# Kernel tuning notes

Hardware: AMD Instinct MI355X
Metric: run time of the kernel (lower is better)

Reference implementation:

```python
import jax, jax.numpy as jnp
import numpy as np

B, T, H, OUT = 256, 512, 512, 256  # batch, seq_len, hidden_size, out_seq_len


def setup_inputs() -> dict:
    key = jax.random.key(0)
    ks = jax.random.split(key, 16)
    sc = 1.0 / np.sqrt(H)  # torch GRU/Linear uniform(-1/sqrt(H),1/sqrt(H)) scale; use scaled normal
    p = lambda k, shape: (jax.random.normal(k, shape, jnp.float32) * sc)
    return {
        "x": jax.random.normal(ks[0], (B, T, 1), jnp.float32),
        # GRU layer 0 (input size 1)
        "W_ih0": p(ks[1], (3 * H, 1)),
        "W_hh0": p(ks[2], (3 * H, H)),
        "b_ih0": p(ks[3], (3 * H,)),
        "b_hh0": p(ks[4], (3 * H,)),
        # GRU layer 1 (input size H)
        "W_ih1": p(ks[5], (3 * H, H)),
        "W_hh1": p(ks[6], (3 * H, H)),
        "b_ih1": p(ks[7], (3 * H,)),
        "b_hh1": p(ks[8], (3 * H,)),
        # FC head: Linear(H,H)+ReLU, Linear(H,H)+ReLU, Linear(H,OUT)+Sigmoid
        "W1": p(ks[9], (H, H)),  "b1": p(ks[10], (H,)),
        "W2": p(ks[11], (H, H)), "b2": p(ks[12], (H,)),
        "W3": p(ks[13], (OUT, H)), "b3": p(ks[14], (OUT,)),
    }


def gru_layer(x, Wih, Whh, bih, bhh):
    # x: [B, T, in]; torch GRU equations (gate order r, z, n)
    gx = jnp.einsum('bti,gi->btg', x, Wih) + bih  # [B, T, 3H], input part precomputed

    def step(h, g):
        gh = h @ Whh.T + bhh                      # [B, 3H]
        xr, xz, xn = jnp.split(g, 3, axis=-1)
        hr, hz, hn = jnp.split(gh, 3, axis=-1)
        r = jax.nn.sigmoid(xr + hr)
        z = jax.nn.sigmoid(xz + hz)
        n = jnp.tanh(xn + r * hn)
        h = (1.0 - z) * n + z * h
        return h, h

    h0 = jnp.zeros((x.shape[0], Whh.shape[1]), x.dtype)
    _, hs = jax.lax.scan(step, h0, jnp.swapaxes(gx, 0, 1))  # [T, B, H]
    return jnp.swapaxes(hs, 0, 1)                            # [B, T, H]


def reference(x, W_ih0, W_hh0, b_ih0, b_hh0, W_ih1, W_hh1, b_ih1, b_hh1,
              W1, b1, W2, b2, W3, b3):
    h = gru_layer(x, W_ih0, W_hh0, b_ih0, b_hh0)
    h = gru_layer(h, W_ih1, W_hh1, b_ih1, b_hh1)
    y = h[:, -1]                                  # last timestep, [B, H]
    y = jax.nn.relu(y @ W1.T + b1)
    y = jax.nn.relu(y @ W2.T + b2)
    y = jax.nn.sigmoid(y @ W3.T + b3)             # [B, OUT]
    return y[..., None]                            # [B, OUT, 1]
```

## Files before the change

### kernel.cpp

```cpp
#include <hip/hip_runtime.h>


#define HSLOT 131072

typedef __attribute__((ext_vector_type(8))) _Float16 f16x8;
typedef __attribute__((ext_vector_type(4))) float f32x4;

__device__ __forceinline__ float sig_(float v) { return 1.0f / (1.0f + expf(-v)); }

__global__ __launch_bounds__(256) void ws_zero_v4(float* __restrict__ h) {
  int i = blockIdx.x * 256 + threadIdx.x;
  for (; i < 4 * HSLOT; i += gridDim.x * 256) h[i] = 0.f;
}

__global__ __launch_bounds__(256) void gru_step_m(
    const float* __restrict__ x,
    const float* __restrict__ Wih0, const float* __restrict__ bih0,
    const float* __restrict__ Whh0, const float* __restrict__ bhh0,
    const float* __restrict__ Wih1, const float* __restrict__ bih1,
    const float* __restrict__ Whh1, const float* __restrict__ bhh1,
    float* __restrict__ h0, float* __restrict__ h1, const int t)
{
  extern __shared__ char lds[];
  const int tid = threadIdx.x;
  const int w = tid >> 6, lane = tid & 63, l15 = lane & 15, q = lane >> 4;
  const bool isL1 = blockIdx.x >= 128;
  const int bb2 = isL1 ? (int)blockIdx.x - 128 : (int)blockIdx.x;
  const int bt = bb2 & 3, dt = bb2 >> 2;
  if (!isL1 && t >= 512) return;
  if (isL1 && t < 1) return;
  const int m0 = bt * 64;
  const int d  = dt * 16 + l15;

  const float* h0prev = h0 + (size_t)((t + 1) & 1) * HSLOT;

  {
    const int NR = isL1 ? 96 : 48;
    for (int u = tid; u < NR * 64; u += 256) {
      const int r = u >> 6, c8 = u & 63;
      const int mat = r >> 6 >= 0 ? (r >= 48 ? 1 : 0) : 0;
      const int rr = r - mat * 48, g3 = rr >> 4, dd = rr & 15;
      const float* W = isL1 ? (mat ? Whh1 : Wih1) : Whh0;
      const float* src = W + (size_t)(g3 * 512 + dt * 16 + dd) * 512 + (c8 << 3);
      const float4 v0 = *(const float4*)src;
      const float4 v1 = *(const float4*)(src + 4);
      f16x8 hv;
      hv[0] = (_Float16)v0.x; hv[1] = (_Float16)v0.y;
      hv[2] = (_Float16)v0.z; hv[3] = (_Float16)v0.w;
      hv[4] = (_Float16)v1.x; hv[5] = (_Float16)v1.y;
      hv[6] = (_Float16)v1.z; hv[7] = (_Float16)v1.w;
      *(f16x8*)(lds + (r << 10) + ((c8 ^ (r & 7)) << 4)) = hv;
    }
  }
  __syncthreads();

  f32x4 acc[6];
  #pragma unroll
  for (int i = 0; i < 6; ++i) acc[i] = (f32x4){0.f, 0.f, 0.f, 0.f};

  const float* h1prev = h1 + (size_t)(t & 1) * HSLOT;
  const size_t arow = (size_t)(m0 + w * 16 + l15) * 512 + (q << 3);

  #pragma unroll
  for (int half = 0; half < 2; ++half) {
    f16x8 a0[8], a1[8];
    #pragma unroll
    for (int kc2 = 0; kc2 < 8; ++kc2) {
      const int kc = half * 8 + kc2;
      const float* ap0 = h0prev + arow + kc * 32;
      const float4 u0 = *(const float4*)ap0, u1 = *(const float4*)(ap0 + 4);
      a0[kc2][0] = (_Float16)u0.x; a0[kc2][1] = (_Float16)u0.y;
      a0[kc2][2] = (_Float16)u0.z; a0[kc2][3] = (_Float16)u0.w;
      a0[kc2][4] = (_Float16)u1.x; a0[kc2][5] = (_Float16)u1.y;
      a0[kc2][6] = (_Float16)u1.z; a0[kc2][7] = (_Float16)u1.w;
      if (isL1) {
        const float* ap1 = h1prev + arow + kc * 32;
        const float4 v0 = *(const float4*)ap1, v1 = *(const float4*)(ap1 + 4);
        a1[kc2][0] = (_Float16)v0.x; a1[kc2][1] = (_Float16)v0.y;
        a1[kc2][2] = (_Float16)v0.z; a1[kc2][3] = (_Float16)v0.w;
        a1[kc2][4] = (_Float16)v1.x; a1[kc2][5] = (_Float16)v1.y;
        a1[kc2][6] = (_Float16)v1.z; a1[kc2][7] = (_Float16)v1.w;
      }
    }
    #pragma unroll
    for (int kc2 = 0; kc2 < 8; ++kc2) {
      const int kc = half * 8 + kc2;
      const int bb = ((kc << 6) + (q << 4)) ^ ((l15 & 7) << 4);
      #pragma unroll
      for (int g3 = 0; g3 < 3; ++g3) {
        const f16x8 bf = *(const f16x8*)(lds + ((g3 * 16 + l15) << 10) + bb);
        acc[g3] = __builtin_amdgcn_mfma_f32_16x16x32_f16(a0[kc2], bf, acc[g3], 0, 0, 0);
      }
      if (isL1) {
        #pragma unroll
        for (int g3 = 0; g3 < 3; ++g3) {
          const f16x8 bf = *(const f16x8*)(lds + 49152 + ((g3 * 16 + l15) << 10) + bb);
          acc[3 + g3] = __builtin_amdgcn_mfma_f32_16x16x32_f16(a1[kc2], bf, acc[3 + g3], 0, 0, 0);
        }
      }
    }
  }

  if (!isL1) {
    const float wxr = Wih0[d], wxz = Wih0[512 + d], wxn = Wih0[1024 + d];
    const float bxr = bih0[d], bxz = bih0[512 + d], bxn = bih0[1024 + d];
    const float bhr = bhh0[d], bhz = bhh0[512 + d], bhn = bhh0[1024 + d];
    float* hdst = h0 + (size_t)(t & 1) * HSLOT;
    #pragma unroll
    for (int j = 0; j < 4; ++j) {
      const int b = m0 + w * 16 + q * 4 + j;
      const float xv = x[(size_t)b * 512 + t];
      const float hp = h0prev[(size_t)b * 512 + d];
      const float r = sig_(xv * wxr + bxr + acc[0][j] + bhr);
      const float z = sig_(xv * wxz + bxz + acc[1][j] + bhz);
      const float n = tanhf(xv * wxn + bxn + r * (acc[2][j] + bhn));
      hdst[(size_t)b * 512 + d] = (1.f - z) * n + z * hp;
    }
  } else {
    const float bxr = bih1[d], bxz = bih1[512 + d], bxn = bih1[1024 + d];
    const float bhr = bhh1[d], bhz = bhh1[512 + d], bhn = bhh1[1024 + d];
    float* hdst = h1 + (size_t)((t + 1) & 1) * HSLOT;
    #pragma unroll
    for (int j = 0; j < 4; ++j) {
      const int b = m0 + w * 16 + q * 4 + j;
      const float hp = h1prev[(size_t)b * 512 + d];
      const float r = sig_(acc[0][j] + bxr + acc[3][j] + bhr);
      const float z = sig_(acc[1][j] + bxz + acc[4][j] + bhz);
      const float n = tanhf(acc[2][j] + bxn + r * (acc[5][j] + bhn));
      hdst[(size_t)b * 512 + d] = (1.f - z) * n + z * hp;
    }
  }
}

__global__ __launch_bounds__(256)
void mlp_head_v4(const float* __restrict__ X, const float* __restrict__ W,
                 const float* __restrict__ bias, float* __restrict__ Y,
                 const int N, const int act)
{
  __shared__ float Xs[32][258];
  __shared__ float Ws[8][260];
  const int tid = threadIdx.x;
  const int m0 = blockIdx.x << 5;
  const int j0 = blockIdx.y << 6;
  const int b  = tid >> 3;
  const int jj = tid & 7;
  float acc[8];
  #pragma unroll
  for (int i = 0; i < 8; ++i) acc[i] = 0.f;
  for (int kh = 0; kh < 2; ++kh) {
    __syncthreads();
    for (int u = tid; u < 2048; u += 256) {
      const int row = u >> 6, c4 = u & 63;
      const float4 v = *((const float4*)(X + ((m0 + row) << 9) + (kh << 8)) + c4);
      float* dst = &Xs[row][c4 << 2];
      dst[0] = v.x; dst[1] = v.y; dst[2] = v.z; dst[3] = v.w;
    }
    __syncthreads();
    #pragma unroll
    for (int jg = 0; jg < 8; ++jg) {
      if (jg) __syncthreads();
      for (int u = tid; u < 512; u += 256) {
        const int row = u >> 6, c4 = u & 63;
        const float4 v = *((const float4*)(W + ((j0 + (jg << 3) + row) << 9) + (kh << 8)) + c4);
        float* dst = &Ws[row][c4 << 2];
        dst[0] = v.x; dst[1] = v.y; dst[2] = v.z; dst[3] = v.w;
      }
      __syncthreads();
      float a = 0.f;
      #pragma unroll 8
      for (int k = 0; k < 256; ++k) a += Xs[b][k] * Ws[jj][k];
      acc[jg] += a;
    }
  }
  #pragma unroll
  for (int jg = 0; jg < 8; ++jg) {
    const int j = j0 + (jg << 3) + jj;
    float v = acc[jg] + bias[j];
    v = act ? (1.f / (1.f + __expf(-v))) : fmaxf(v, 0.f);
    Y[(m0 + b) * N + j] = v;
  }
}

extern "C" void kernel_launch(void* const* d_in, const int* in_sizes, int n_in,
                              void* d_out, int out_size, void* d_ws, size_t ws_size,
                              hipStream_t stream) {
  (void)in_sizes; (void)n_in; (void)out_size; (void)ws_size;
  const float* x    = (const float*)d_in[0];
  const float* Wih0 = (const float*)d_in[1];
  const float* Whh0 = (const float*)d_in[2];
  const float* bih0 = (const float*)d_in[3];
  const float* bhh0 = (const float*)d_in[4];
  const float* Wih1 = (const float*)d_in[5];
  const float* Whh1 = (const float*)d_in[6];
  const float* bih1 = (const float*)d_in[7];
  const float* bhh1 = (const float*)d_in[8];
  const float* W1 = (const float*)d_in[9];
  const float* b1 = (const float*)d_in[10];
  const float* W2 = (const float*)d_in[11];
  const float* b2 = (const float*)d_in[12];
  const float* W3 = (const float*)d_in[13];
  const float* b3 = (const float*)d_in[14];

  float* h0 = (float*)d_ws;
  float* h1 = h0 + 2 * HSLOT;
  float* y1 = h1 + 2 * HSLOT;
  float* y2 = y1 + HSLOT;

  hipFuncSetAttribute((const void*)gru_step_m,
                      hipFuncAttributeMaxDynamicSharedMemorySize, 98304);

  ws_zero_v4<<<64, 256, 0, stream>>>(h0);
  for (int t = 0; t <= 512; ++t)
    gru_step_m<<<256, 256, 98304, stream>>>(x, Wih0, bih0, Whh0, bhh0,
                                            Wih1, bih1, Whh1, bhh1, h0, h1, t);
  mlp_head_v4<<<dim3(8, 8), 256, 0, stream>>>(h1 + HSLOT, W1, b1, y1, 512, 0);
  mlp_head_v4<<<dim3(8, 8), 256, 0, stream>>>(y1, W2, b2, y2, 512, 0);
  mlp_head_v4<<<dim3(8, 4), 256, 0, stream>>>(y2, W3, b3, (float*)d_out, 256, 1);
}
```

Measured before the change: 10.81 ms.

## Replace per-timestep launches with persistent cooperative GRU kernel and grid barrier

Swaps 513 separate step launches for one cooperative persistent kernel of 192 blocks, each synchronised per timestep by a hierarchical atomic grid barrier. Work is split into three roles: layer0 recurrence, layer1 input projection (pipelined one step ahead through a gx buffer), and layer1 recurrence. Weights stay resident in LDS across all steps and hidden state is kept in registers, while the exchanged state is stored as fp16, which halves state traffic and removes conversions. The risks are the latency of a spin barrier on every step and extra fp16 rounding of the shared hidden state.

```diff
diff --git a/kernel.cpp b/kernel.cpp
--- a/kernel.cpp
+++ b/kernel.cpp
@@ -1,47 +1,56 @@
 #include <hip/hip_runtime.h>
 
 
-#define HSLOT 131072
+#define NTH 512
 
 typedef __attribute__((ext_vector_type(8))) _Float16 f16x8;
 typedef __attribute__((ext_vector_type(4))) float f32x4;
 
+__device__ __forceinline__ unsigned short f2h(float f) {
+  union { _Float16 h; unsigned short u; } v; v.h = (_Float16)f;
+  return v.u;
+}
 __device__ __forceinline__ float sig_(float v) { return 1.0f / (1.0f + expf(-v)); }
 
-__global__ __launch_bounds__(256) void ws_zero_v4(float* __restrict__ h) {
+__global__ __launch_bounds__(256) void ws_zero_v5(unsigned* __restrict__ p) {
   int i = blockIdx.x * 256 + threadIdx.x;
-  for (; i < 4 * HSLOT; i += gridDim.x * 256) h[i] = 0.f;
-}
-
-__global__ __launch_bounds__(256) void gru_step_m(
+  for (; i < 262144; i += gridDim.x * 256) p[i] = 0u;
+}
+
+__global__ __launch_bounds__(NTH, 1) void gru_persist(
     const float* __restrict__ x,
-    const float* __restrict__ Wih0, const float* __restrict__ bih0,
-    const float* __restrict__ Whh0, const float* __restrict__ bhh0,
-    const float* __restrict__ Wih1, const float* __restrict__ bih1,
-    const float* __restrict__ Whh1, const float* __restrict__ bhh1,
-    float* __restrict__ h0, float* __restrict__ h1, const int t)
+    const float* __restrict__ Wih0, const float* __restrict__ Whh0,
+    const float* __restrict__ bih0, const float* __restrict__ bhh0,
+    const float* __restrict__ Wih1, const float* __restrict__ Whh1,
+    const float* __restrict__ bih1, const float* __restrict__ bhh1,
+    char* __restrict__ ws, float* __restrict__ h1f)
 {
   extern __shared__ char lds[];
+
+  unsigned* cnt = (unsigned*)ws;
+  unsigned* gen = (unsigned*)(ws + 512);
+  unsigned short* h0b = (unsigned short*)(ws + 4096);
+  unsigned short* h1b = h0b + 2 * 131072;
+  float* gxb = (float*)(ws + 1052672);
+
   const int tid = threadIdx.x;
-  const int w = tid >> 6, lane = tid & 63, l15 = lane & 15, q = lane >> 4;
-  const bool isL1 = blockIdx.x >= 128;
-  const int bb2 = isL1 ? (int)blockIdx.x - 128 : (int)blockIdx.x;
-  const int bt = bb2 & 3, dt = bb2 >> 2;
-  if (!isL1 && t >= 512) return;
-  if (isL1 && t < 1) return;
-  const int m0 = bt * 64;
-  const int d  = dt * 16 + l15;
-
-  const float* h0prev = h0 + (size_t)((t + 1) & 1) * HSLOT;
+  const int wv = tid >> 6, lane = tid & 63, l15 = lane & 15, q = lane >> 4;
+  const int bid = blockIdx.x;
+  const int role = bid >> 6;
+  const int rb = bid & 63;
+  const int bt = rb & 3, dt = rb >> 2;
+  const int rg = wv >> 1;
+  const int hh = wv & 1;
+  const int row0 = bt * 64 + rg * 16;
+  const int dim = dt * 32 + hh * 16 + l15;
+  const int swl = (l15 & 7) << 4;
 
   {
-    const int NR = isL1 ? 96 : 48;
-    for (int u = tid; u < NR * 64; u += 256) {
+    const float* Wsrc = role == 0 ? Whh0 : (role == 1 ? Wih1 : Whh1);
+    for (int u = tid; u < 96 * 64; u += NTH) {
       const int r = u >> 6, c8 = u & 63;
-      const int mat = r >> 6 >= 0 ? (r >= 48 ? 1 : 0) : 0;
-      const int rr = r - mat * 48, g3 = rr >> 4, dd = rr & 15;
-      const float* W = isL1 ? (mat ? Whh1 : Wih1) : Whh0;
-      const float* src = W + (size_t)(g3 * 512 + dt * 16 + dd) * 512 + (c8 << 3);
+      const int g3 = r >> 5, dd = r & 31;
+      const float* src = Wsrc + (size_t)((g3 << 9) + dt * 32 + dd) * 512 + (c8 << 3);
       const float4 v0 = *(const float4*)src;
       const float4 v1 = *(const float4*)(src + 4);
       f16x8 hv;
@@ -52,88 +61,127 @@
       *(f16x8*)(lds + (r << 10) + ((c8 ^ (r & 7)) << 4)) = hv;
     }
   }
+
+  float c0w[3], c0i[3], c0h[3], c1i[3], c1h[3];
+  if (role == 0) {
+    #pragma unroll
+    for (int g3 = 0; g3 < 3; ++g3) {
+      c0w[g3] = Wih0[(g3 << 9) + dim];
+      c0i[g3] = bih0[(g3 << 9) + dim];
+      c0h[g3] = bhh0[(g3 << 9) + dim];
+    }
+  } else if (role == 2) {
+    #pragma unroll
+    for (int g3 = 0; g3 < 3; ++g3) {
+      c1i[g3] = bih1[(g3 << 9) + dim];
+      c1h[g3] = bhh1[(g3 << 9) + dim];
+    }
+  }
+
+  float hst[4];
+  #pragma unroll
+  for (int j = 0; j < 4; ++j) hst[j] = 0.f;
+
   __syncthreads();
 
-  f32x4 acc[6];
-  #pragma unroll
-  for (int i = 0; i < 6; ++i) acc[i] = (f32x4){0.f, 0.f, 0.f, 0.f};
-
-  const float* h1prev = h1 + (size_t)(t & 1) * HSLOT;
-  const size_t arow = (size_t)(m0 + w * 16 + l15) * 512 + (q << 3);
-
-  #pragma unroll
-  for (int half = 0; half < 2; ++half) {
-    f16x8 a0[8], a1[8];
-    #pragma unroll
-    for (int kc2 = 0; kc2 < 8; ++kc2) {
-      const int kc = half * 8 + kc2;
-      const float* ap0 = h0prev + arow + kc * 32;
-      const float4 u0 = *(const float4*)ap0, u1 = *(const float4*)(ap0 + 4);
-      a0[kc2][0] = (_Float16)u0.x; a0[kc2][1] = (_Float16)u0.y;
-      a0[kc2][2] = (_Float16)u0.z; a0[kc2][3] = (_Float16)u0.w;
-      a0[kc2][4] = (_Float16)u1.x; a0[kc2][5] = (_Float16)u1.y;
-      a0[kc2][6] = (_Float16)u1.z; a0[kc2][7] = (_Float16)u1.w;
-      if (isL1) {
-        const float* ap1 = h1prev + arow + kc * 32;
-        const float4 v0 = *(const float4*)ap1, v1 = *(const float4*)(ap1 + 4);
-        a1[kc2][0] = (_Float16)v0.x; a1[kc2][1] = (_Float16)v0.y;
-        a1[kc2][2] = (_Float16)v0.z; a1[kc2][3] = (_Float16)v0.w;
-        a1[kc2][4] = (_Float16)v1.x; a1[kc2][5] = (_Float16)v1.y;
-        a1[kc2][6] = (_Float16)v1.z; a1[kc2][7] = (_Float16)v1.w;
-      }
-    }
-    #pragma unroll
-    for (int kc2 = 0; kc2 < 8; ++kc2) {
-      const int kc = half * 8 + kc2;
-      const int bb = ((kc << 6) + (q << 4)) ^ ((l15 & 7) << 4);
+  for (int t = 0; t <= 513; ++t) {
+    const bool act = (role == 0) ? (t < 512)
+                   : (role == 1) ? (t >= 1 && t <= 512)
+                                 : (t >= 2);
+    f32x4 acc[3];
+    #pragma unroll
+    for (int g3 = 0; g3 < 3; ++g3) acc[g3] = (f32x4){0.f, 0.f, 0.f, 0.f};
+
+    if (act) {
+      const unsigned short* hsrc =
+          (role == 2 ? h1b : h0b) + (size_t)((t + 1) & 1) * 131072;
+      const unsigned short* ap = hsrc + (size_t)(row0 + l15) * 512 + (q << 3);
       #pragma unroll
-      for (int g3 = 0; g3 < 3; ++g3) {
-        const f16x8 bf = *(const f16x8*)(lds + ((g3 * 16 + l15) << 10) + bb);
-        acc[g3] = __builtin_amdgcn_mfma_f32_16x16x32_f16(a0[kc2], bf, acc[g3], 0, 0, 0);
-      }
-      if (isL1) {
-        #pragma unroll
-        for (int g3 = 0; g3 < 3; ++g3) {
-          const f16x8 bf = *(const f16x8*)(lds + 49152 + ((g3 * 16 + l15) << 10) + bb);
-          acc[3 + g3] = __builtin_amdgcn_mfma_f32_16x16x32_f16(a1[kc2], bf, acc[3 + g3], 0, 0, 0);
+      for (int half = 0; half < 2; ++half) {
+        f16x8 af[8];
+        #pragma unroll
+        for (int kc2 = 0; kc2 < 8; ++kc2)
+          af[kc2] = *(const f16x8*)(ap + (half * 8 + kc2) * 32);
+        #pragma unroll
+        for (int kc2 = 0; kc2 < 8; ++kc2) {
+          const int kc = half * 8 + kc2;
+          const int bb = ((kc << 6) + (q << 4)) ^ swl;
+          #pragma unroll
+          for (int g3 = 0; g3 < 3; ++g3) {
+            const f16x8 bf = *(const f16x8*)(lds + (((g3 << 5) + (hh << 4) + l15) << 10) + bb);
+            acc[g3] = __builtin_amdgcn_mfma_f32_16x16x32_f16(af[kc2], bf, acc[g3], 0, 0, 0);
+          }
         }
       }
     }
-  }
-
-  if (!isL1) {
-    const float wxr = Wih0[d], wxz = Wih0[512 + d], wxn = Wih0[1024 + d];
-    const float bxr = bih0[d], bxz = bih0[512 + d], bxn = bih0[1024 + d];
-    const float bhr = bhh0[d], bhz = bhh0[512 + d], bhn = bhh0[1024 + d];
-    float* hdst = h0 + (size_t)(t & 1) * HSLOT;
-    #pragma unroll
-    for (int j = 0; j < 4; ++j) {
-      const int b = m0 + w * 16 + q * 4 + j;
-      const float xv = x[(size_t)b * 512 + t];
-      const float hp = h0prev[(size_t)b * 512 + d];
-      const float r = sig_(xv * wxr + bxr + acc[0][j] + bhr);
-      const float z = sig_(xv * wxz + bxz + acc[1][j] + bhz);
-      const float n = tanhf(xv * wxn + bxn + r * (acc[2][j] + bhn));
-      hdst[(size_t)b * 512 + d] = (1.f - z) * n + z * hp;
-    }
-  } else {
-    const float bxr = bih1[d], bxz = bih1[512 + d], bxn = bih1[1024 + d];
-    const float bhr = bhh1[d], bhz = bhh1[512 + d], bhn = bhh1[1024 + d];
-    float* hdst = h1 + (size_t)((t + 1) & 1) * HSLOT;
-    #pragma unroll
-    for (int j = 0; j < 4; ++j) {
-      const int b = m0 + w * 16 + q * 4 + j;
-      const float hp = h1prev[(size_t)b * 512 + d];
-      const float r = sig_(acc[0][j] + bxr + acc[3][j] + bhr);
-      const float z = sig_(acc[1][j] + bxz + acc[4][j] + bhz);
-      const float n = tanhf(acc[2][j] + bxn + r * (acc[5][j] + bhn));
-      hdst[(size_t)b * 512 + d] = (1.f - z) * n + z * hp;
-    }
+
+    if (act) {
+      if (role == 0) {
+        unsigned short* hdst = h0b + (size_t)(t & 1) * 131072;
+        #pragma unroll
+        for (int j = 0; j < 4; ++j) {
+          const int row = row0 + q * 4 + j;
+          const float xv = x[(size_t)row * 512 + t];
+          const float r = sig_(xv * c0w[0] + c0i[0] + acc[0][j] + c0h[0]);
+          const float z = sig_(xv * c0w[1] + c0i[1] + acc[1][j] + c0h[1]);
+          const float n = tanhf(xv * c0w[2] + c0i[2] + r * (acc[2][j] + c0h[2]));
+          const float h = (1.f - z) * n + z * hst[j];
+          hst[j] = h;
+          hdst[(size_t)row * 512 + dim] = f2h(h);
+        }
+      } else if (role == 1) {
+        float* gxc = gxb + (size_t)(((t + 1) & 1) * 64 + rb) * 6144;
+        #pragma unroll
+        for (int g3 = 0; g3 < 3; ++g3)
+          #pragma unroll
+          for (int j = 0; j < 4; ++j)
+            gxc[(rg * 16 + q * 4 + j) * 96 + (g3 << 5) + (hh << 4) + l15] = acc[g3][j];
+      } else {
+        const float* gxc = gxb + (size_t)((t & 1) * 64 + rb) * 6144;
+        unsigned short* hdst = h1b + (size_t)(t & 1) * 131072;
+        #pragma unroll
+        for (int j = 0; j < 4; ++j) {
+          const int rr = rg * 16 + q * 4 + j;
+          const float gxr = gxc[rr * 96 + (hh << 4) + l15];
+          const float gxz = gxc[rr * 96 + 32 + (hh << 4) + l15];
+          const float gxn = gxc[rr * 96 + 64 + (hh << 4) + l15];
+          const float r = sig_(gxr + c1i[0] + acc[0][j] + c1h[0]);
+          const float z = sig_(gxz + c1i[1] + acc[1][j] + c1h[1]);
+          const float n = tanhf(gxn + c1i[2] + r * (acc[2][j] + c1h[2]));
+          const float h = (1.f - z) * n + z * hst[j];
+          hst[j] = h;
+          const int row = row0 + q * 4 + j;
+          hdst[(size_t)row * 512 + dim] = f2h(h);
+          if (t == 513) h1f[(size_t)row * 512 + dim] = h;
+        }
+      }
+    }
+
+    __syncthreads();
+    if (tid == 0) {
+      __hip_atomic_fetch_add(&cnt[(bid & 7) << 4], 1u,
+                             __ATOMIC_RELEASE, __HIP_MEMORY_SCOPE_AGENT);
+      const unsigned tgt = 24u * (unsigned)(t + 1);
+      if (bid == 0) {
+        for (int i = 0; i < 8; ++i)
+          while (__hip_atomic_load(&cnt[i << 4], __ATOMIC_ACQUIRE,
+                                   __HIP_MEMORY_SCOPE_AGENT) < tgt)
+            __builtin_amdgcn_s_sleep(2);
+        __hip_atomic_store(gen, (unsigned)(t + 1),
+                           __ATOMIC_RELEASE, __HIP_MEMORY_SCOPE_AGENT);
+      } else {
+        while (__hip_atomic_load(gen, __ATOMIC_ACQUIRE,
+                                 __HIP_MEMORY_SCOPE_AGENT) < (unsigned)(t + 1))
+          __builtin_amdgcn_s_sleep(2);
+      }
+    }
+    __syncthreads();
+    __builtin_amdgcn_sched_barrier(0);
   }
 }
 
 __global__ __launch_bounds__(256)
-void mlp_head_v4(const float* __restrict__ X, const float* __restrict__ W,
+void mlp_head_v5(const float* __restrict__ X, const float* __restrict__ W,
                  const float* __restrict__ bias, float* __restrict__ Y,
                  const int N, const int act)
 {
@@ -201,19 +249,25 @@
   const float* W3 = (const float*)d_in[13];
   const float* b3 = (const float*)d_in[14];
 
-  float* h0 = (float*)d_ws;
-  float* h1 = h0 + 2 * HSLOT;
-  float* y1 = h1 + 2 * HSLOT;
-  float* y2 = y1 + HSLOT;
-
-  hipFuncSetAttribute((const void*)gru_step_m,
+  char* ws = (char*)d_ws;
+  float* h1f = (float*)(ws + 4198400);
+  float* y1  = (float*)(ws + 4722688);
+  float* y2  = (float*)(ws + 5246976);
+
+  hipMemsetAsync(ws, 0, 4096, stream);
+  ws_zero_v5<<<64, 256, 0, stream>>>((unsigned*)(ws + 4096));
+
+  hipFuncSetAttribute((const void*)gru_persist,
                       hipFuncAttributeMaxDynamicSharedMemorySize, 98304);
 
-  ws_zero_v4<<<64, 256, 0, stream>>>(h0);
-  for (int t = 0; t <= 512; ++t)
-    gru_step_m<<<256, 256, 98304, stream>>>(x, Wih0, bih0, Whh0, bhh0,
-                                            Wih1, bih1, Whh1, bhh1, h0, h1, t);
-  mlp_head_v4<<<dim3(8, 8), 256, 0, stream>>>(h1 + HSLOT, W1, b1, y1, 512, 0);
-  mlp_head_v4<<<dim3(8, 8), 256, 0, stream>>>(y1, W2, b2, y2, 512, 0);
-  mlp_head_v4<<<dim3(8, 4), 256, 0, stream>>>(y2, W3, b3, (float*)d_out, 256, 1);
-}
+  void* args[11];
+  args[0] = &x;    args[1] = &Wih0; args[2] = &Whh0; args[3] = &bih0;
+  args[4] = &bhh0; args[5] = &Wih1; args[6] = &Whh1; args[7] = &bih1;
+  args[8] = &bhh1; args[9] = &ws;   args[10] = &h1f;
+  hipLaunchCooperativeKernel((const void*)gru_persist, dim3(192), dim3(NTH),
+                             args, 98304, stream);
+
+  mlp_head_v5<<<dim3(8, 8), 256, 0, stream>>>(h1f, W1, b1, y1, 512, 0);
+  mlp_head_v5<<<dim3(8, 8), 256, 0, stream>>>(y1, W2, b2, y2, 512, 0);
+  mlp_head_v5<<<dim3(8, 4), 256, 0, stream>>>(y2, W3, b3, (float*)d_out, 256, 1);
+}
```

Result: slower. 14.60 ms (+35.1%).
